# Performance work log

Measured on AMD Instinct MI355X. Metric: run time of the kernel, lower is better.

The kernel has to match this reference:

```python
import jax, jax.numpy as jnp
import numpy as np
from jax import lax


def _conv3x3(x, w):
    # x: [B, Cin, V, T], w: [Cout, Cin, 3, 3]; stride 1, padding 1, no bias
    return lax.conv_general_dilated(x, w, window_strides=(1, 1), padding='SAME',
                                    dimension_numbers=('NCHW', 'OIHW', 'NCHW'))


def setup_inputs() -> dict:
    key = jax.random.key(0)
    ks = jax.random.split(key, 5)
    B, C, V, T = 8, 128, 256, 128
    Cqk, Cv = C // 8, C // 2
    x = jax.random.normal(ks[0], (B, C, V, T), dtype=jnp.float32)
    s = 0.05
    Wq = jax.random.normal(ks[1], (Cqk, C, 3, 3), dtype=jnp.float32) * s
    Wk = jax.random.normal(ks[2], (Cqk, C, 3, 3), dtype=jnp.float32) * s
    Wv = jax.random.normal(ks[3], (Cv, C, 3, 3), dtype=jnp.float32) * s
    Wav = jax.random.normal(ks[4], (C, Cv, 3, 3), dtype=jnp.float32) * s
    sigma = jnp.array([0.5], dtype=jnp.float32)
    return {"x": x, "Wq": Wq, "Wk": Wk, "Wv": Wv, "Wav": Wav, "sigma": sigma}


def reference(x, Wq, Wk, Wv, Wav, sigma):
    # Projections (3x3 convs), tanh on Q and K
    q = jnp.tanh(_conv3x3(x, Wq))   # [B, Cqk, V, T]
    k = jnp.tanh(_conv3x3(x, Wk))   # [B, Cqk, V, T]
    v = _conv3x3(x, Wv)             # [B, Cv,  V, T]
    # Per-(b,t) attention over V: scores[b,t,v,w] = sum_c q[b,c,v,t] k[b,c,w,t]
    scores = jnp.einsum('bcvt,bcwt->btvw', q, k)
    attn = jax.nn.softmax(scores, axis=-1)
    av = jnp.einsum('btvw,bcwt->bcvt', attn, v)  # [B, Cv, V, T]
    out = _conv3x3(av, Wav)                      # [B, C, V, T]
    return x + sigma[0] * out
```

## Files before the change

### kernel.cpp

```cpp
#include <hip/hip_runtime.h>
#include <hip/hip_bf16.h>

#define B_  8
#define C_  128
#define V_  256
#define T_  128
#define CQK 16
#define CV  64
#define CO1 96
#define VP  (V_ + 2)
#define TP  (T_ + 2)

typedef __attribute__((ext_vector_type(8)))  short short8;
typedef __attribute__((ext_vector_type(4)))  short s16x4;
typedef __attribute__((ext_vector_type(4)))  float f32x4;
typedef __attribute__((ext_vector_type(16))) float f32x16;
typedef __attribute__((ext_vector_type(4)))  unsigned int u32x4;

#define L2E   1.44269504f
#define EXPB  23.0831204f

#define XP_BYTES   (B_ * VP * TP * C_ * 2)
#define AVP_BYTES  (B_ * VP * TP * CV * 2)
#define QKV_OFF    XP_BYTES
#define QKV_BYTES  (B_ * V_ * T_ * CO1 * 2)
#define WQKV_OFF   (QKV_OFF + QKV_BYTES)
#define WQKV_BYTES (9 * CO1 * C_ * 2)
#define WAV_OFF    (WQKV_OFF + WQKV_BYTES)
#define WAV_BYTES  (9 * C_ * CV * 2)

__device__ __forceinline__ void gload_lds16(const void* g, void* l) {
    __builtin_amdgcn_global_load_lds((const __attribute__((address_space(1))) void*)g,
                                     (__attribute__((address_space(3))) void*)l,
                                     16, 0, 0);
}

__global__ __launch_bounds__(256) void zero_halo(__hip_bfloat16* __restrict__ p, int CH) {
    const int b = blockIdx.y;
    const int nrow = 2 * TP * CH;
    const int ncol = (VP - 2) * 2 * CH;
    const __hip_bfloat16 z = __float2bfloat16(0.f);
    for (int e = blockIdx.x * 256 + threadIdx.x; e < nrow + ncol; e += gridDim.x * 256) {
        size_t off;
        if (e < nrow) {
            const int r = e / (TP * CH), k = e % (TP * CH);
            off = (((size_t)b * VP + (size_t)r * (VP - 1)) * TP) * CH + k;
        } else {
            const int e2 = e - nrow;
            const int v = e2 / (2 * CH) + 1, k2 = e2 % (2 * CH);
            const int t = (k2 < CH) ? 0 : (TP - 1);
            const int c = k2 & (CH - 1);
            off = (((size_t)b * VP + v) * TP + t) * CH + c;
        }
        p[off] = z;
    }
}

__global__ __launch_bounds__(256) void pack_x_kernel(const float* __restrict__ x,
                                                     __hip_bfloat16* __restrict__ xp) {
    __shared__ __hip_bfloat16 tile[T_ * (C_ + 1)];
    const int v = blockIdx.x, b = blockIdx.y, tid = threadIdx.x;

    for (int e = tid; e < C_ * T_; e += 256) {
        const int c = e >> 7, t = e & (T_ - 1);
        tile[t * (C_ + 1) + c] =
            __float2bfloat16(x[(((size_t)b * C_ + c) * V_ + v) * T_ + t]);
    }
    __syncthreads();
    __hip_bfloat16* dst = xp + (((size_t)b * VP + (v + 1)) * TP + 1) * C_;
    for (int e = tid; e < C_ * T_; e += 256) {
        const int t = e >> 7, c = e & (C_ - 1);
        dst[(size_t)t * C_ + c] = tile[t * (C_ + 1) + c];
    }
}

__global__ void pack_w_kernel(const float* __restrict__ Wq, const float* __restrict__ Wk,
                              const float* __restrict__ Wv, const float* __restrict__ Wav,
                              __hip_bfloat16* __restrict__ wqkvp,
                              __hip_bfloat16* __restrict__ wavp) {
    const int tid = blockIdx.x * blockDim.x + threadIdx.x;
    const int n1 = 9 * CO1 * C_;
    const int n2 = 9 * C_ * CV;
    for (int e = tid; e < n1 + n2; e += gridDim.x * blockDim.x) {
        if (e < n1) {
            const int s = e / (CO1 * C_), r = e % (CO1 * C_);
            const int co = r / C_, ci = r % C_;
            const int dy = s / 3, dx = s % 3;
            float w;
            if (co < CQK)            w = Wq[(((size_t)co * C_ + ci) * 3 + dy) * 3 + dx];
            else if (co < 2 * CQK)   w = Wk[(((size_t)(co - CQK) * C_ + ci) * 3 + dy) * 3 + dx];
            else                     w = Wv[(((size_t)(co - 2 * CQK) * C_ + ci) * 3 + dy) * 3 + dx];
            const int sw = ((co * 256 + ci * 2) ^ ((co & 7) << 4)) >> 1;
            wqkvp[s * (CO1 * C_) + sw] = __float2bfloat16(w);
        } else {
            const int e2 = e - n1;
            const int s = e2 / (C_ * CV), r = e2 % (C_ * CV);
            const int co = r / CV, ci = r % CV;
            const int dy = s / 3, dx = s % 3;
            const int sw = ((co * 128 + ci * 2) ^ ((co & 7) << 4)) >> 1;
            wavp[s * (C_ * CV) + sw] =
                __float2bfloat16(Wav[(((size_t)co * CV + ci) * 3 + dy) * 3 + dx]);
        }
    }
}

__global__ __launch_bounds__(256, 2) void conv_qkv_mfma(const __hip_bfloat16* __restrict__ xp,
                                                        const __hip_bfloat16* __restrict__ wqkvp,
                                                        __hip_bfloat16* __restrict__ qkv) {
    __shared__ __align__(16) char wlds[2][24576];
    const int flat = blockIdx.x + (blockIdx.y << 8);
    const int y = flat >> 3, b = flat & 7;
    const int tid = threadIdx.x;
    const int wave = tid >> 6, lane = tid & 63;
    const int lane16 = lane & 15, lgrp = lane >> 4;
    const int t0w = wave * 32;

    const char* wbase = (const char*)wqkvp;

    f32x4 acc[6][2];
    #pragma unroll
    for (int m = 0; m < 6; ++m)
        #pragma unroll
        for (int n = 0; n < 2; ++n) acc[m][n] = (f32x4){0.f, 0.f, 0.f, 0.f};

    short8 bfr[2][4][2];
    {
        const char* gsrc = wbase + wave * 6144 + lane * 16;
        char* ldst = &wlds[0][wave * 6144];
        #pragma unroll
        for (int j = 0; j < 6; ++j)
            gload_lds16(gsrc + j * 1024, ldst + j * 1024);
        const __hip_bfloat16* xrow = xp + (((size_t)b * VP + y) * TP + 0) * C_;
        #pragma unroll
        for (int kk = 0; kk < 4; ++kk)
            #pragma unroll
            for (int nt = 0; nt < 2; ++nt)
                bfr[0][kk][nt] = *reinterpret_cast<const short8*>(
                    xrow + (size_t)(t0w + nt * 16 + lane16) * C_ + kk * 32 + lgrp * 8);
    }
    __syncthreads();

    const int kb6   = (lane16 & 4) << 4;
    const int lbase = lane16 * 256 + ((lgrp * 16) ^ ((lane16 & 3) << 4));

    #pragma unroll
    for (int s = 0; s < 9; ++s) {
        const int cur = s & 1, nxt = cur ^ 1;
        if (s < 8) {
            const char* gsrc = wbase + (s + 1) * 24576 + wave * 6144 + lane * 16;
            char* ldst = &wlds[nxt][wave * 6144];
            #pragma unroll
            for (int j = 0; j < 6; ++j)
                gload_lds16(gsrc + j * 1024, ldst + j * 1024);
            const int dy = (s + 1) / 3, dx = (s + 1) % 3;
            const __hip_bfloat16* xrow = xp + (((size_t)b * VP + (y + dy)) * TP + dx) * C_;
            #pragma unroll
            for (int kk = 0; kk < 4; ++kk)
                #pragma unroll
                for (int nt = 0; nt < 2; ++nt)
                    bfr[nxt][kk][nt] = *reinterpret_cast<const short8*>(
                        xrow + (size_t)(t0w + nt * 16 + lane16) * C_ + kk * 32 + lgrp * 8);
            __builtin_amdgcn_sched_barrier(0);
        }
        const char* wcur = &wlds[cur][0];
        #pragma unroll
        for (int kk = 0; kk < 4; ++kk) {
            const int koff = lbase + ((kk * 64) ^ kb6);
            #pragma unroll
            for (int m = 0; m < 6; ++m) {
                const short8 afrag = *reinterpret_cast<const short8*>(wcur + koff + m * 4096);
                acc[m][0] = __builtin_amdgcn_mfma_f32_16x16x32_bf16(afrag, bfr[cur][kk][0], acc[m][0], 0, 0, 0);
                acc[m][1] = __builtin_amdgcn_mfma_f32_16x16x32_bf16(afrag, bfr[cur][kk][1], acc[m][1], 0, 0, 0);
            }
        }
        __syncthreads();
    }

    unsigned short* tl = (unsigned short*)&wlds[0][0];
    #pragma unroll
    for (int m = 0; m < 6; ++m) {
        const int co = m * 16 + lgrp * 4;
        #pragma unroll
        for (int nt = 0; nt < 2; ++nt) {
            const int t = t0w + nt * 16 + lane16;
            s16x4 pk4;
            #pragma unroll
            for (int r = 0; r < 4; ++r) {
                float v = acc[m][nt][r];
                if (co + r < 2 * CQK) {
                    v = tanhf(v);
                    if (co + r < CQK) v *= L2E;
                }
                pk4[r] = __builtin_bit_cast(short, __float2bfloat16(v));
            }
            *reinterpret_cast<s16x4*>(&tl[t * 104 + co]) = pk4;
        }
    }
    __syncthreads();
    {
        const int t = tid >> 1, half = tid & 1;
        const unsigned short* src = &tl[t * 104 + half * 48];
        __hip_bfloat16* dst = qkv + (((size_t)b * T_ + t) * V_ + y) * CO1 + half * 48;
        #pragma unroll
        for (int j = 0; j < 6; ++j)
            *reinterpret_cast<short8*>(dst + j * 8) =
                *reinterpret_cast<const short8*>(src + j * 8);
    }
}

__global__ __launch_bounds__(256) void attn_mfma(const __hip_bfloat16* __restrict__ qkv,
                                                 __hip_bfloat16* __restrict__ avp) {
    __shared__ short qf[8][64][8];
    __shared__ short kf[8][64][8];
    __shared__ short vf[32][64][8];

    const int t   = blockIdx.x & (T_ - 1);
    const int b   = blockIdx.x >> 7;
    const int tid = threadIdx.x;
    const int lane = tid & 63, wid = tid >> 6;
    const int l31 = lane & 31, hi = lane >> 5;

    const __hip_bfloat16* base = qkv + ((size_t)b * T_ + t) * (V_ * CO1);

    #pragma unroll
    for (int pass = 0; pass < 2; ++pass) {
        const int idx = tid + pass * 256;
        const int w = idx >> 1, h = idx & 1;
        const int ls = (w & 31) | (h << 5);
        const short8 qv = *reinterpret_cast<const short8*>(base + (size_t)w * CO1 + h * 8);
        const short8 kv = *reinterpret_cast<const short8*>(base + (size_t)w * CO1 + CQK + h * 8);
        *reinterpret_cast<short8*>(&qf[w >> 5][ls][0]) = qv;
        *reinterpret_cast<short8*>(&kf[w >> 5][ls][0]) = kv;
    }
    {
        const int c = tid & 63, wg = tid >> 6;
        const int ct = c >> 5, c31 = c & 31;
        #pragma unroll
        for (int pass = 0; pass < 8; ++pass) {
            const int w0 = (pass * 4 + wg) * 8;
            short8 vv;
            #pragma unroll
            for (int i = 0; i < 8; ++i)
                vv[i] = *reinterpret_cast<const short*>(base + (size_t)(w0 + i) * CO1 + 2 * CQK + c);
            const int ls = c31 | (((w0 >> 3) & 1) << 5);
            *reinterpret_cast<short8*>(&vf[(w0 >> 4) * 2 + ct][ls][0]) = vv;
        }
    }
    __syncthreads();

    #pragma unroll
    for (int sp = 0; sp < 2; ++sp) {
        const int strip = wid * 2 + sp;
        const short8 bq = *reinterpret_cast<const short8*>(&qf[strip][lane][0]);

        f32x16 o0, o1;
        #pragma unroll
        for (int r = 0; r < 16; ++r) { o0[r] = 0.f; o1[r] = 0.f; }
        float lsum = 0.f;

        for (int wt = 0; wt < 8; ++wt) {
            const short8 ak = *reinterpret_cast<const short8*>(&kf[wt][lane][0]);
            f32x16 st;
            #pragma unroll
            for (int r = 0; r < 16; ++r) st[r] = -EXPB;
            st = __builtin_amdgcn_mfma_f32_32x32x16_bf16(ak, bq, st, 0, 0, 0);

            float p[16];
            #pragma unroll
            for (int r = 0; r < 16; ++r) { p[r] = __builtin_exp2f(st[r]); lsum += p[r]; }

            unsigned pk[8], xpk[8];
            #pragma unroll
            for (int i = 0; i < 8; ++i) {
                const unsigned lo  = __builtin_bit_cast(unsigned short, __float2bfloat16(p[2 * i]));
                const unsigned hiw = __builtin_bit_cast(unsigned short, __float2bfloat16(p[2 * i + 1]));
                pk[i] = lo | (hiw << 16);
            }
            #pragma unroll
            for (int i = 0; i < 8; ++i) xpk[i] = __shfl_xor(pk[i], 32);

            const u32x4 fa0 = hi ? (u32x4){xpk[2], xpk[3], pk[2], pk[3]}
                                 : (u32x4){pk[0], pk[1], xpk[0], xpk[1]};
            const u32x4 fa1 = hi ? (u32x4){xpk[6], xpk[7], pk[6], pk[7]}
                                 : (u32x4){pk[4], pk[5], xpk[4], xpk[5]};
            const short8 a0 = __builtin_bit_cast(short8, fa0);
            const short8 a1 = __builtin_bit_cast(short8, fa1);

            const short8 v00 = *reinterpret_cast<const short8*>(&vf[wt * 4 + 0][lane][0]);
            const short8 v01 = *reinterpret_cast<const short8*>(&vf[wt * 4 + 1][lane][0]);
            const short8 v10 = *reinterpret_cast<const short8*>(&vf[wt * 4 + 2][lane][0]);
            const short8 v11 = *reinterpret_cast<const short8*>(&vf[wt * 4 + 3][lane][0]);

            o0 = __builtin_amdgcn_mfma_f32_32x32x16_bf16(a0, v00, o0, 0, 0, 0);
            o1 = __builtin_amdgcn_mfma_f32_32x32x16_bf16(a0, v01, o1, 0, 0, 0);
            o0 = __builtin_amdgcn_mfma_f32_32x32x16_bf16(a1, v10, o0, 0, 0, 0);
            o1 = __builtin_amdgcn_mfma_f32_32x32x16_bf16(a1, v11, o1, 0, 0, 0);
        }

        lsum += __shfl_xor(lsum, 32);
        const float rl = 1.f / lsum;

        const size_t obase = (((size_t)b * VP) * TP + (t + 1)) * CV;
        #pragma unroll
        for (int r = 0; r < 16; ++r) {
            const int row = (r & 3) + 8 * (r >> 2) + 4 * hi;
            const float rlr = __shfl(rl, row);
            __hip_bfloat16* op = avp + obase + (size_t)(strip * 32 + row + 1) * ((size_t)TP * CV) + l31;
            op[0]  = __float2bfloat16(o0[r] * rlr);
            op[32] = __float2bfloat16(o1[r] * rlr);
        }
    }
}

__global__ __launch_bounds__(256) void conv_out_mfma(const float* __restrict__ x,
                                                     const __hip_bfloat16* __restrict__ avp,
                                                     const __hip_bfloat16* __restrict__ wavp,
                                                     const float* __restrict__ sigma,
                                                     float* __restrict__ out) {
    __shared__ __align__(16) char wlds[2][16384];
    const int flat = blockIdx.x + (blockIdx.y << 8);
    const int y = flat >> 3, b = flat & 7;
    const int tid = threadIdx.x;
    const int wave = tid >> 6, lane = tid & 63;
    const int lane16 = lane & 15, lgrp = lane >> 4;
    const int t0w = wave * 32;
    const float sig = sigma[0];

    const char* wbase = (const char*)wavp;

    f32x4 acc[8][2];
    #pragma unroll
    for (int m = 0; m < 8; ++m)
        #pragma unroll
        for (int n = 0; n < 2; ++n) acc[m][n] = (f32x4){0.f, 0.f, 0.f, 0.f};

    short8 bfr[2][2][2];
    {
        const char* gsrc = wbase + wave * 4096 + lane * 16;
        char* ldst = &wlds[0][wave * 4096];
        #pragma unroll
        for (int j = 0; j < 4; ++j)
            gload_lds16(gsrc + j * 1024, ldst + j * 1024);
        const __hip_bfloat16* arow = avp + (((size_t)b * VP + y) * TP + 0) * CV;
        #pragma unroll
        for (int kk = 0; kk < 2; ++kk)
            #pragma unroll
            for (int nt = 0; nt < 2; ++nt)
                bfr[0][kk][nt] = *reinterpret_cast<const short8*>(
                    arow + (size_t)(t0w + nt * 16 + lane16) * CV + kk * 32 + lgrp * 8);
    }
    __syncthreads();

    const int kb6   = (lane16 & 4) << 4;
    const int lbase = lane16 * 128 + ((lgrp * 16) ^ ((lane16 & 3) << 4));

    #pragma unroll
    for (int s = 0; s < 9; ++s) {
        const int cur = s & 1, nxt = cur ^ 1;
        if (s < 8) {
            const char* gsrc = wbase + (s + 1) * 16384 + wave * 4096 + lane * 16;
            char* ldst = &wlds[nxt][wave * 4096];
            #pragma unroll
            for (int j = 0; j < 4; ++j)
                gload_lds16(gsrc + j * 1024, ldst + j * 1024);
            const int dy = (s + 1) / 3, dx = (s + 1) % 3;
            const __hip_bfloat16* arow = avp + (((size_t)b * VP + (y + dy)) * TP + dx) * CV;
            #pragma unroll
            for (int kk = 0; kk < 2; ++kk)
                #pragma unroll
                for (int nt = 0; nt < 2; ++nt)
                    bfr[nxt][kk][nt] = *reinterpret_cast<const short8*>(
                        arow + (size_t)(t0w + nt * 16 + lane16) * CV + kk * 32 + lgrp * 8);
        }
        const char* wcur = &wlds[cur][0];
        #pragma unroll
        for (int kk = 0; kk < 2; ++kk) {
            const int koff = lbase + ((kk * 64) ^ kb6);
            #pragma unroll
            for (int m = 0; m < 8; ++m) {
                const short8 afrag = *reinterpret_cast<const short8*>(wcur + koff + m * 2048);
                acc[m][0] = __builtin_amdgcn_mfma_f32_16x16x32_bf16(afrag, bfr[cur][kk][0], acc[m][0], 0, 0, 0);
                acc[m][1] = __builtin_amdgcn_mfma_f32_16x16x32_bf16(afrag, bfr[cur][kk][1], acc[m][1], 0, 0, 0);
            }
        }
        __syncthreads();
    }

    float* tl = (float*)&wlds[0][0];
    const int co_q = tid >> 3;
    const int tt0  = (tid & 7) * 16;
    #pragma unroll
    for (int p = 0; p < 4; ++p) {
        #pragma unroll
        for (int mm = 0; mm < 2; ++mm) {
            const int m  = p * 2 + mm;
            const int cl = mm * 16 + lgrp * 4;
            #pragma unroll
            for (int nt = 0; nt < 2; ++nt) {
                const int t = t0w + nt * 16 + lane16;
                #pragma unroll
                for (int r = 0; r < 4; ++r)
                    tl[(cl + r) * 132 + t] = acc[m][nt][r];
            }
        }
        __syncthreads();
        const int co = p * 32 + co_q;
        const float* xs = x   + (((size_t)b * C_ + co) * V_ + y) * T_ + tt0;
        float*       os = out + (((size_t)b * C_ + co) * V_ + y) * T_ + tt0;
        #pragma unroll
        for (int j = 0; j < 4; ++j) {
            const f32x4 xv = *reinterpret_cast<const f32x4*>(xs + j * 4);
            const f32x4 cv = *reinterpret_cast<const f32x4*>(&tl[co_q * 132 + tt0 + j * 4]);
            f32x4 ov;
            ov[0] = xv[0] + sig * cv[0];
            ov[1] = xv[1] + sig * cv[1];
            ov[2] = xv[2] + sig * cv[2];
            ov[3] = xv[3] + sig * cv[3];
            *reinterpret_cast<f32x4*>(os + j * 4) = ov;
        }
        if (p < 3) __syncthreads();
    }
}

extern "C" void kernel_launch(void* const* d_in, const int* in_sizes, int n_in,
                              void* d_out, int out_size, void* d_ws, size_t ws_size,
                              hipStream_t stream) {
    const float* x     = (const float*)d_in[0];
    const float* Wq    = (const float*)d_in[1];
    const float* Wk    = (const float*)d_in[2];
    const float* Wv    = (const float*)d_in[3];
    const float* Wav   = (const float*)d_in[4];
    const float* sigma = (const float*)d_in[5];
    float* out = (float*)d_out;

    char* wsp = (char*)d_ws;
    __hip_bfloat16* xp    = (__hip_bfloat16*)wsp;
    __hip_bfloat16* avp   = (__hip_bfloat16*)wsp;
    __hip_bfloat16* qkv   = (__hip_bfloat16*)(wsp + QKV_OFF);
    __hip_bfloat16* wqkvp = (__hip_bfloat16*)(wsp + WQKV_OFF);
    __hip_bfloat16* wavp  = (__hip_bfloat16*)(wsp + WAV_OFF);

    zero_halo<<<dim3(64, B_), dim3(256), 0, stream>>>(xp, C_);
    pack_x_kernel<<<dim3(V_, B_), dim3(256), 0, stream>>>(x, xp);
    pack_w_kernel<<<dim3(32), dim3(256), 0, stream>>>(Wq, Wk, Wv, Wav, wqkvp, wavp);
    conv_qkv_mfma<<<dim3(V_, B_), dim3(256), 0, stream>>>(xp, wqkvp, qkv);
    zero_halo<<<dim3(64, B_), dim3(256), 0, stream>>>(avp, CV);
    attn_mfma<<<dim3(B_ * T_), dim3(256), 0, stream>>>(qkv, avp);
    conv_out_mfma<<<dim3(V_, B_), dim3(256), 0, stream>>>(x, avp, wavp, sigma, out);
}
```

Baseline: 278.5 us.

## Process two output rows per block in both convs to reuse staged weights

Both conv kernels now have each block compute two adjacent V rows, with waves split two by two across rows and T halves. Each wave covers 64 T positions with 4 N-tiles, so each LDS weight fragment feeds twice as many MFMAs. This halves the weight staging traffic per output and the grid size. The register prefetch of activation fragments for the next tap is dropped, so loads now happen just before use, and the larger accumulator arrays raise register pressure. The output conv also gains a two-blocks-per-CU launch bound.

Result: slower. 327.7 us (+17.7%).

```diff
diff --git a/kernel.cpp b/kernel.cpp
--- a/kernel.cpp
+++ b/kernel.cpp
@@ -108,36 +108,29 @@
                                                         const __hip_bfloat16* __restrict__ wqkvp,
                                                         __hip_bfloat16* __restrict__ qkv) {
     __shared__ __align__(16) char wlds[2][24576];
-    const int flat = blockIdx.x + (blockIdx.y << 8);
-    const int y = flat >> 3, b = flat & 7;
+    const int flat = blockIdx.x;
+    const int b = flat & 7, y0 = (flat >> 3) * 2;
     const int tid = threadIdx.x;
     const int wave = tid >> 6, lane = tid & 63;
     const int lane16 = lane & 15, lgrp = lane >> 4;
-    const int t0w = wave * 32;
+    const int yw = wave >> 1, th = wave & 1;
+    const int y = y0 + yw;
+    const int t0w = th * 64;
 
     const char* wbase = (const char*)wqkvp;
-
-    f32x4 acc[6][2];
-    #pragma unroll
-    for (int m = 0; m < 6; ++m)
-        #pragma unroll
-        for (int n = 0; n < 2; ++n) acc[m][n] = (f32x4){0.f, 0.f, 0.f, 0.f};
-
-    short8 bfr[2][4][2];
     {
         const char* gsrc = wbase + wave * 6144 + lane * 16;
         char* ldst = &wlds[0][wave * 6144];
         #pragma unroll
         for (int j = 0; j < 6; ++j)
             gload_lds16(gsrc + j * 1024, ldst + j * 1024);
-        const __hip_bfloat16* xrow = xp + (((size_t)b * VP + y) * TP + 0) * C_;
-        #pragma unroll
-        for (int kk = 0; kk < 4; ++kk)
-            #pragma unroll
-            for (int nt = 0; nt < 2; ++nt)
-                bfr[0][kk][nt] = *reinterpret_cast<const short8*>(
-                    xrow + (size_t)(t0w + nt * 16 + lane16) * C_ + kk * 32 + lgrp * 8);
-    }
+    }
+
+    f32x4 acc[6][4];
+    #pragma unroll
+    for (int m = 0; m < 6; ++m)
+        #pragma unroll
+        for (int n = 0; n < 4; ++n) acc[m][n] = (f32x4){0.f, 0.f, 0.f, 0.f};
     __syncthreads();
 
     const int kb6   = (lane16 & 4) << 4;
@@ -152,16 +145,16 @@
             #pragma unroll
             for (int j = 0; j < 6; ++j)
                 gload_lds16(gsrc + j * 1024, ldst + j * 1024);
-            const int dy = (s + 1) / 3, dx = (s + 1) % 3;
-            const __hip_bfloat16* xrow = xp + (((size_t)b * VP + (y + dy)) * TP + dx) * C_;
-            #pragma unroll
-            for (int kk = 0; kk < 4; ++kk)
-                #pragma unroll
-                for (int nt = 0; nt < 2; ++nt)
-                    bfr[nxt][kk][nt] = *reinterpret_cast<const short8*>(
-                        xrow + (size_t)(t0w + nt * 16 + lane16) * C_ + kk * 32 + lgrp * 8);
-            __builtin_amdgcn_sched_barrier(0);
-        }
+        }
+        const int dy = s / 3, dx = s % 3;
+        const __hip_bfloat16* xrow = xp + (((size_t)b * VP + (y + dy)) * TP + dx) * C_;
+        short8 bfr[4][4];
+        #pragma unroll
+        for (int kk = 0; kk < 4; ++kk)
+            #pragma unroll
+            for (int nt = 0; nt < 4; ++nt)
+                bfr[kk][nt] = *reinterpret_cast<const short8*>(
+                    xrow + (size_t)(t0w + nt * 16 + lane16) * C_ + kk * 32 + lgrp * 8);
         const char* wcur = &wlds[cur][0];
         #pragma unroll
         for (int kk = 0; kk < 4; ++kk) {
@@ -169,8 +162,9 @@
             #pragma unroll
             for (int m = 0; m < 6; ++m) {
                 const short8 afrag = *reinterpret_cast<const short8*>(wcur + koff + m * 4096);
-                acc[m][0] = __builtin_amdgcn_mfma_f32_16x16x32_bf16(afrag, bfr[cur][kk][0], acc[m][0], 0, 0, 0);
-                acc[m][1] = __builtin_amdgcn_mfma_f32_16x16x32_bf16(afrag, bfr[cur][kk][1], acc[m][1], 0, 0, 0);
+                #pragma unroll
+                for (int nt = 0; nt < 4; ++nt)
+                    acc[m][nt] = __builtin_amdgcn_mfma_f32_16x16x32_bf16(afrag, bfr[kk][nt], acc[m][nt], 0, 0, 0);
             }
         }
         __syncthreads();
@@ -178,33 +172,39 @@
 
     unsigned short* tl = (unsigned short*)&wlds[0][0];
     #pragma unroll
-    for (int m = 0; m < 6; ++m) {
-        const int co = m * 16 + lgrp * 4;
-        #pragma unroll
-        for (int nt = 0; nt < 2; ++nt) {
-            const int t = t0w + nt * 16 + lane16;
-            s16x4 pk4;
-            #pragma unroll
-            for (int r = 0; r < 4; ++r) {
-                float v = acc[m][nt][r];
-                if (co + r < 2 * CQK) {
-                    v = tanhf(v);
-                    if (co + r < CQK) v *= L2E;
+    for (int pass = 0; pass < 2; ++pass) {
+        if (yw == pass) {
+            #pragma unroll
+            for (int m = 0; m < 6; ++m) {
+                const int co = m * 16 + lgrp * 4;
+                #pragma unroll
+                for (int nt = 0; nt < 4; ++nt) {
+                    const int t = t0w + nt * 16 + lane16;
+                    s16x4 pk4;
+                    #pragma unroll
+                    for (int r = 0; r < 4; ++r) {
+                        float v = acc[m][nt][r];
+                        if (co + r < 2 * CQK) {
+                            v = tanhf(v);
+                            if (co + r < CQK) v *= L2E;
+                        }
+                        pk4[r] = __builtin_bit_cast(short, __float2bfloat16(v));
+                    }
+                    *reinterpret_cast<s16x4*>(&tl[t * 104 + co]) = pk4;
                 }
-                pk4[r] = __builtin_bit_cast(short, __float2bfloat16(v));
-            }
-            *reinterpret_cast<s16x4*>(&tl[t * 104 + co]) = pk4;
-        }
-    }
-    __syncthreads();
-    {
-        const int t = tid >> 1, half = tid & 1;
-        const unsigned short* src = &tl[t * 104 + half * 48];
-        __hip_bfloat16* dst = qkv + (((size_t)b * T_ + t) * V_ + y) * CO1 + half * 48;
-        #pragma unroll
-        for (int j = 0; j < 6; ++j)
-            *reinterpret_cast<short8*>(dst + j * 8) =
-                *reinterpret_cast<const short8*>(src + j * 8);
+            }
+        }
+        __syncthreads();
+        {
+            const int t = tid >> 1, half = tid & 1;
+            const unsigned short* src = &tl[t * 104 + half * 48];
+            __hip_bfloat16* dst = qkv + (((size_t)b * T_ + t) * V_ + (y0 + pass)) * CO1 + half * 48;
+            #pragma unroll
+            for (int j = 0; j < 6; ++j)
+                *reinterpret_cast<short8*>(dst + j * 8) =
+                    *reinterpret_cast<const short8*>(src + j * 8);
+        }
+        if (pass == 0) __syncthreads();
     }
 }
 
@@ -312,43 +312,36 @@
     }
 }
 
-__global__ __launch_bounds__(256) void conv_out_mfma(const float* __restrict__ x,
-                                                     const __hip_bfloat16* __restrict__ avp,
-                                                     const __hip_bfloat16* __restrict__ wavp,
-                                                     const float* __restrict__ sigma,
-                                                     float* __restrict__ out) {
+__global__ __launch_bounds__(256, 2) void conv_out_mfma(const float* __restrict__ x,
+                                                        const __hip_bfloat16* __restrict__ avp,
+                                                        const __hip_bfloat16* __restrict__ wavp,
+                                                        const float* __restrict__ sigma,
+                                                        float* __restrict__ out) {
     __shared__ __align__(16) char wlds[2][16384];
-    const int flat = blockIdx.x + (blockIdx.y << 8);
-    const int y = flat >> 3, b = flat & 7;
+    const int flat = blockIdx.x;
+    const int b = flat & 7, y0 = (flat >> 3) * 2;
     const int tid = threadIdx.x;
     const int wave = tid >> 6, lane = tid & 63;
     const int lane16 = lane & 15, lgrp = lane >> 4;
-    const int t0w = wave * 32;
+    const int yw = wave >> 1, th = wave & 1;
+    const int y = y0 + yw;
+    const int t0w = th * 64;
     const float sig = sigma[0];
 
     const char* wbase = (const char*)wavp;
-
-    f32x4 acc[8][2];
-    #pragma unroll
-    for (int m = 0; m < 8; ++m)
-        #pragma unroll
-        for (int n = 0; n < 2; ++n) acc[m][n] = (f32x4){0.f, 0.f, 0.f, 0.f};
-
-    short8 bfr[2][2][2];
     {
         const char* gsrc = wbase + wave * 4096 + lane * 16;
         char* ldst = &wlds[0][wave * 4096];
         #pragma unroll
         for (int j = 0; j < 4; ++j)
             gload_lds16(gsrc + j * 1024, ldst + j * 1024);
-        const __hip_bfloat16* arow = avp + (((size_t)b * VP + y) * TP + 0) * CV;
-        #pragma unroll
-        for (int kk = 0; kk < 2; ++kk)
-            #pragma unroll
-            for (int nt = 0; nt < 2; ++nt)
-                bfr[0][kk][nt] = *reinterpret_cast<const short8*>(
-                    arow + (size_t)(t0w + nt * 16 + lane16) * CV + kk * 32 + lgrp * 8);
-    }
+    }
+
+    f32x4 acc[8][4];
+    #pragma unroll
+    for (int m = 0; m < 8; ++m)
+        #pragma unroll
+        for (int n = 0; n < 4; ++n) acc[m][n] = (f32x4){0.f, 0.f, 0.f, 0.f};
     __syncthreads();
 
     const int kb6   = (lane16 & 4) << 4;
@@ -363,15 +356,16 @@
             #pragma unroll
             for (int j = 0; j < 4; ++j)
                 gload_lds16(gsrc + j * 1024, ldst + j * 1024);
-            const int dy = (s + 1) / 3, dx = (s + 1) % 3;
-            const __hip_bfloat16* arow = avp + (((size_t)b * VP + (y + dy)) * TP + dx) * CV;
-            #pragma unroll
-            for (int kk = 0; kk < 2; ++kk)
-                #pragma unroll
-                for (int nt = 0; nt < 2; ++nt)
-                    bfr[nxt][kk][nt] = *reinterpret_cast<const short8*>(
-                        arow + (size_t)(t0w + nt * 16 + lane16) * CV + kk * 32 + lgrp * 8);
-        }
+        }
+        const int dy = s / 3, dx = s % 3;
+        const __hip_bfloat16* arow = avp + (((size_t)b * VP + (y + dy)) * TP + dx) * CV;
+        short8 bfr[2][4];
+        #pragma unroll
+        for (int kk = 0; kk < 2; ++kk)
+            #pragma unroll
+            for (int nt = 0; nt < 4; ++nt)
+                bfr[kk][nt] = *reinterpret_cast<const short8*>(
+                    arow + (size_t)(t0w + nt * 16 + lane16) * CV + kk * 32 + lgrp * 8);
         const char* wcur = &wlds[cur][0];
         #pragma unroll
         for (int kk = 0; kk < 2; ++kk) {
@@ -379,8 +373,9 @@
             #pragma unroll
             for (int m = 0; m < 8; ++m) {
                 const short8 afrag = *reinterpret_cast<const short8*>(wcur + koff + m * 2048);
-                acc[m][0] = __builtin_amdgcn_mfma_f32_16x16x32_bf16(afrag, bfr[cur][kk][0], acc[m][0], 0, 0, 0);
-                acc[m][1] = __builtin_amdgcn_mfma_f32_16x16x32_bf16(afrag, bfr[cur][kk][1], acc[m][1], 0, 0, 0);
+                #pragma unroll
+                for (int nt = 0; nt < 4; ++nt)
+                    acc[m][nt] = __builtin_amdgcn_mfma_f32_16x16x32_bf16(afrag, bfr[kk][nt], acc[m][nt], 0, 0, 0);
             }
         }
         __syncthreads();
@@ -390,35 +385,40 @@
     const int co_q = tid >> 3;
     const int tt0  = (tid & 7) * 16;
     #pragma unroll
-    for (int p = 0; p < 4; ++p) {
-        #pragma unroll
-        for (int mm = 0; mm < 2; ++mm) {
-            const int m  = p * 2 + mm;
-            const int cl = mm * 16 + lgrp * 4;
-            #pragma unroll
-            for (int nt = 0; nt < 2; ++nt) {
-                const int t = t0w + nt * 16 + lane16;
+    for (int yy = 0; yy < 2; ++yy) {
+        #pragma unroll
+        for (int p = 0; p < 4; ++p) {
+            if (yw == yy) {
                 #pragma unroll
-                for (int r = 0; r < 4; ++r)
-                    tl[(cl + r) * 132 + t] = acc[m][nt][r];
-            }
-        }
-        __syncthreads();
-        const int co = p * 32 + co_q;
-        const float* xs = x   + (((size_t)b * C_ + co) * V_ + y) * T_ + tt0;
-        float*       os = out + (((size_t)b * C_ + co) * V_ + y) * T_ + tt0;
-        #pragma unroll
-        for (int j = 0; j < 4; ++j) {
-            const f32x4 xv = *reinterpret_cast<const f32x4*>(xs + j * 4);
-            const f32x4 cv = *reinterpret_cast<const f32x4*>(&tl[co_q * 132 + tt0 + j * 4]);
-            f32x4 ov;
-            ov[0] = xv[0] + sig * cv[0];
-            ov[1] = xv[1] + sig * cv[1];
-            ov[2] = xv[2] + sig * cv[2];
-            ov[3] = xv[3] + sig * cv[3];
-            *reinterpret_cast<f32x4*>(os + j * 4) = ov;
-        }
-        if (p < 3) __syncthreads();
+                for (int mm = 0; mm < 2; ++mm) {
+                    const int m  = p * 2 + mm;
+                    const int cl = mm * 16 + lgrp * 4;
+                    #pragma unroll
+                    for (int nt = 0; nt < 4; ++nt) {
+                        const int t = t0w + nt * 16 + lane16;
+                        #pragma unroll
+                        for (int r = 0; r < 4; ++r)
+                            tl[(cl + r) * 132 + t] = acc[m][nt][r];
+                    }
+                }
+            }
+            __syncthreads();
+            const int co = p * 32 + co_q;
+            const float* xs = x   + (((size_t)b * C_ + co) * V_ + (y0 + yy)) * T_ + tt0;
+            float*       os = out + (((size_t)b * C_ + co) * V_ + (y0 + yy)) * T_ + tt0;
+            #pragma unroll
+            for (int j = 0; j < 4; ++j) {
+                const f32x4 xv = *reinterpret_cast<const f32x4*>(xs + j * 4);
+                const f32x4 cv = *reinterpret_cast<const f32x4*>(&tl[co_q * 132 + tt0 + j * 4]);
+                f32x4 ov;
+                ov[0] = xv[0] + sig * cv[0];
+                ov[1] = xv[1] + sig * cv[1];
+                ov[2] = xv[2] + sig * cv[2];
+                ov[3] = xv[3] + sig * cv[3];
+                *reinterpret_cast<f32x4*>(os + j * 4) = ov;
+            }
+            if (!(yy == 1 && p == 3)) __syncthreads();
+        }
     }
 }
 
@@ -443,8 +443,8 @@
     zero_halo<<<dim3(64, B_), dim3(256), 0, stream>>>(xp, C_);
     pack_x_kernel<<<dim3(V_, B_), dim3(256), 0, stream>>>(x, xp);
     pack_w_kernel<<<dim3(32), dim3(256), 0, stream>>>(Wq, Wk, Wv, Wav, wqkvp, wavp);
-    conv_qkv_mfma<<<dim3(V_, B_), dim3(256), 0, stream>>>(xp, wqkvp, qkv);
+    conv_qkv_mfma<<<dim3(B_ * V_ / 2), dim3(256), 0, stream>>>(xp, wqkvp, qkv);
     zero_halo<<<dim3(64, B_), dim3(256), 0, stream>>>(avp, CV);
     attn_mfma<<<dim3(B_ * T_), dim3(256), 0, stream>>>(qkv, avp);
-    conv_out_mfma<<<dim3(V_, B_), dim3(256), 0, stream>>>(x, avp, wavp, sigma, out);
-}
+    conv_out_mfma<<<dim3(B_ * V_ / 2), dim3(256), 0, stream>>>(x, avp, wavp, sigma, out);
+}
```
